# Performance work log

Hardware: AMD Instinct MI355X
Metric: run time of the kernel (lower is better)

Reference implementation:

```python
import jax, jax.numpy as jnp
import numpy as np

TEMPERATURE = 0.07
SCALE_BY_TEMPERATURE = True
N = 4096
D = 256
N_POS = 32768
CHUNK = 128  # row-chunk size for the cdist to bound the [CHUNK, N, D] temp


def setup_inputs() -> dict:
    key = jax.random.key(0)
    k1, k2, k3 = jax.random.split(key, 3)
    out = jax.random.normal(k1, (N, D), dtype=jnp.float32)
    row = jax.random.randint(k2, (N_POS,), 0, N, dtype=jnp.int32)
    col = jax.random.randint(k3, (N_POS,), 0, N, dtype=jnp.int32)
    return {"out": out, "row": row, "col": col}


def _l1_cdist(x):
    """Pairwise Manhattan distance [N, N], computed in row chunks so the
    [CHUNK, N, D] broadcast temporary stays bounded."""
    n, d = x.shape
    xr = x.reshape(n // CHUNK, CHUNK, d)

    def chunk_dist(xc):  # xc: [CHUNK, D] -> [CHUNK, N]
        return jnp.sum(jnp.abs(xc[:, None, :] - x[None, :, :]), axis=-1)

    return jax.lax.map(chunk_dist, xr).reshape(n, n)


def reference(out, row, col):
    n = out.shape[0]
    sim = -_l1_cdist(out) / TEMPERATURE                      # [N, N]
    logits_max = jax.lax.stop_gradient(jnp.max(sim, axis=1, keepdims=True))
    sim = sim - logits_max
    logits_mask = 1.0 - jnp.eye(n, dtype=sim.dtype)          # zero out self-sims
    denom = jnp.log(jnp.sum(jnp.exp(sim) * logits_mask, axis=1, keepdims=True))
    log_probs = sim - denom                                  # [N, N]
    loss = -jnp.mean(log_probs[row, col])                    # gather positive pairs
    if SCALE_BY_TEMPERATURE:
        loss = loss * TEMPERATURE
    return loss
```

## Files before the change

### kernel.cpp

```cpp
#include <hip/hip_runtime.h>
#include <math.h>

#define N 4096
#define D 256
#define NPOS 32768
#define TEMP 0.07f
#define INVT (1.0f / 0.07f)
#define BIGF 3.0e38f

#define RQ 5.5f
#define QS (255.0f / (2.0f * RQ))
#define DEQ (2.0f * RQ / 255.0f)

#define NT 64
#define NTRI (NT * (NT + 1) / 2)
#define KC 16

#define WS_PSTAT 0
#define WS_T    (2 * N * NT)
#define WS_ACC  (2 * N * NT + N)
#define WS_CNT  (2 * N * NT + N + 1)
#define WS_XQ   (2 * N * NT + N + 4)

__device__ __forceinline__ void sad_acc(unsigned a, unsigned b, unsigned& c) {
#if __has_builtin(__builtin_amdgcn_sad_u8)
    c = __builtin_amdgcn_sad_u8(a, b, c);
#else
    asm("v_sad_u8 %0, %1, %2, %0" : "+v"(c) : "v"(a), "v"(b));
#endif
}

__device__ __forceinline__ void g2l16(const unsigned* g, unsigned* l) {
    __builtin_amdgcn_global_load_lds(
        (const __attribute__((address_space(1))) unsigned*)g,
        (__attribute__((address_space(3))) unsigned*)l, 16, 0, 0);
}

__device__ __forceinline__ unsigned quant1(float v) {
    const float f = fminf(fmaxf((v + RQ) * QS, 0.0f), 255.0f);
    return (unsigned)__float2uint_rn(f);
}

__global__ __launch_bounds__(256)
void cvt_init_k(const float* __restrict__ x, unsigned* __restrict__ xqT,
                float* __restrict__ acc, unsigned* __restrict__ cnt) {
    __shared__ unsigned t[64][65];
    const int r0 = blockIdx.x * 64;
    const int tid = threadIdx.x;
#pragma unroll
    for (int k = 0; k < 16; ++k) {
        const int idx = k * 256 + tid;
        const int rr = idx >> 6;
        const int w = idx & 63;
        const float4 v = ((const float4*)x)[(size_t)(r0 + rr) * 64 + w];
        t[w][rr] = quant1(v.x) | (quant1(v.y) << 8) |
                   (quant1(v.z) << 16) | (quant1(v.w) << 24);
    }
    __syncthreads();
#pragma unroll
    for (int k = 0; k < 16; ++k) {
        const int idx = k * 256 + tid;
        const int w = idx >> 6;
        const int rr = idx & 63;
        xqT[(size_t)w * N + r0 + rr] = t[w][rr];
    }
    if (blockIdx.x == 0 && tid == 0) { *acc = 0.0f; *cnt = 0u; }
}

__global__ __launch_bounds__(64) __attribute__((amdgpu_waves_per_eu(1, 2)))
void dist_tile_k(const unsigned* __restrict__ xqT, float2* __restrict__ pstat) {
    const int tt = blockIdx.x;
    const int u_ = (NTRI - 1) - tt;
    int r = (int)((sqrtf((float)(8 * u_ + 1)) - 1.0f) * 0.5f);
    while (r * (r + 1) / 2 > u_) --r;
    while ((r + 1) * (r + 2) / 2 <= u_) ++r;
    const int bm = (NT - 1) - r;
    const int bn = (NT - 1) - (u_ - r * (r + 1) / 2);
    const bool diag = (bm == bn);

    const int lane = threadIdx.x;
    const int tx = lane & 7;
    const int ty = lane >> 3;

    __shared__ unsigned As[2][KC][64];
    __shared__ unsigned Bs[2][KC][64];

    unsigned uacc[8][8];
#pragma unroll
    for (int i = 0; i < 8; ++i)
#pragma unroll
        for (int j = 0; j < 8; ++j) uacc[i][j] = 0u;

    const int rowA0 = bm * 64;
    const int rowB0 = bn * 64;

    const int lrow = lane >> 4;
    const int lcol = (lane & 15) * 4;
    const unsigned* gA = xqT + (size_t)lrow * N + rowA0 + lcol;
    const unsigned* gB = xqT + (size_t)lrow * N + rowB0 + lcol;

#pragma unroll
    for (int q = 0; q < 4; ++q) {
        g2l16(gA + (size_t)q * 4 * N, &As[0][q * 4][0]);
        g2l16(gB + (size_t)q * 4 * N, &Bs[0][q * 4][0]);
    }
    __syncthreads();

#pragma unroll 1
    for (int chk = 0; chk < 4; ++chk) {
        const int b = chk & 1;
        if (chk < 3) {
            const unsigned* pa = gA + (size_t)(chk + 1) * 16 * N;
            const unsigned* pb = gB + (size_t)(chk + 1) * 16 * N;
            unsigned* Ad = &As[b ^ 1][0][0];
            unsigned* Bd = &Bs[b ^ 1][0][0];
#pragma unroll
            for (int q = 0; q < 4; ++q) {
                g2l16(pa + (size_t)q * 4 * N, Ad + q * 256);
                g2l16(pb + (size_t)q * 4 * N, Bd + q * 256);
            }
        }

        const unsigned* Ab = &As[b][0][0];
        const unsigned* Bb = &Bs[b][0][0];
#pragma unroll
        for (int k4 = 0; k4 < KC; ++k4) {
            const uint4 a0 = *(const uint4*)(Ab + k4 * 64 + ty * 8);
            const uint4 a1 = *(const uint4*)(Ab + k4 * 64 + ty * 8 + 4);
            const uint4 b0 = *(const uint4*)(Bb + k4 * 64 + tx * 8);
            const uint4 b1 = *(const uint4*)(Bb + k4 * 64 + tx * 8 + 4);
            const unsigned av[8] = {a0.x, a0.y, a0.z, a0.w,
                                    a1.x, a1.y, a1.z, a1.w};
            const unsigned bv[8] = {b0.x, b0.y, b0.z, b0.w,
                                    b1.x, b1.y, b1.z, b1.w};
#pragma unroll
            for (int i = 0; i < 8; ++i)
#pragma unroll
                for (int j = 0; j < 8; ++j)
                    sad_acc(av[i], bv[j], uacc[i][j]);
        }
        __syncthreads();
    }

    float acc[8][8];
#pragma unroll
    for (int i = 0; i < 8; ++i)
#pragma unroll
        for (int j = 0; j < 8; ++j)
            acc[i][j] = (float)uacc[i][j] * DEQ;

    if (diag) {
#pragma unroll
        for (int i = 0; i < 8; ++i)
#pragma unroll
            for (int j = 0; j < 8; ++j)
                if (ty * 8 + i == tx * 8 + j)
                    acc[i][j] = BIGF;
    }

#pragma unroll
    for (int i = 0; i < 8; ++i) {
        float mn = BIGF;
#pragma unroll
        for (int j = 0; j < 8; ++j) mn = fminf(mn, acc[i][j]);
        mn = fminf(mn, __shfl_xor(mn, 1, 64));
        mn = fminf(mn, __shfl_xor(mn, 2, 64));
        mn = fminf(mn, __shfl_xor(mn, 4, 64));
        float s = 0.0f;
#pragma unroll
        for (int j = 0; j < 8; ++j)
            s += __expf((mn - acc[i][j]) * INVT);
        s += __shfl_xor(s, 1, 64);
        s += __shfl_xor(s, 2, 64);
        s += __shfl_xor(s, 4, 64);
        if (tx == 0)
            pstat[(size_t)(rowA0 + ty * 8 + i) * NT + bn] = make_float2(mn, s);
    }

    if (!diag) {
#pragma unroll
        for (int j = 0; j < 8; ++j) {
            float mn = BIGF;
#pragma unroll
            for (int i = 0; i < 8; ++i) mn = fminf(mn, acc[i][j]);
            mn = fminf(mn, __shfl_xor(mn, 8, 64));
            mn = fminf(mn, __shfl_xor(mn, 16, 64));
            mn = fminf(mn, __shfl_xor(mn, 32, 64));
            float s = 0.0f;
#pragma unroll
            for (int i = 0; i < 8; ++i)
                s += __expf((mn - acc[i][j]) * INVT);
            s += __shfl_xor(s, 8, 64);
            s += __shfl_xor(s, 16, 64);
            s += __shfl_xor(s, 32, 64);
            if (ty == 0)
                pstat[(size_t)(rowB0 + tx * 8 + j) * NT + bm] =
                    make_float2(mn, s);
        }
    }
}

__global__ __launch_bounds__(256)
void row_stats_k(const float2* __restrict__ pstat, float* __restrict__ t) {
    const int r = blockIdx.x * 4 + (threadIdx.x >> 6);
    const int c = threadIdx.x & 63;
    const float2 p = pstat[(size_t)r * NT + c];
    float mn = p.x;
#pragma unroll
    for (int off = 32; off > 0; off >>= 1) mn = fminf(mn, __shfl_xor(mn, off, 64));
    float s = p.y * __expf((mn - p.x) * INVT);
#pragma unroll
    for (int off = 32; off > 0; off >>= 1) s += __shfl_xor(s, off, 64);
    if (c == 0) t[r] = TEMP * __logf(s) - mn;
}

__global__ __launch_bounds__(256)
void pair_fin_k(const float* __restrict__ x, const int* __restrict__ row,
                const int* __restrict__ col, const float* __restrict__ t,
                float* __restrict__ acc, unsigned* __restrict__ cnt,
                float* __restrict__ out) {
    const int lane = threadIdx.x & 63;
    const int wave = threadIdx.x >> 6;
    const int p0 = (blockIdx.x * 4 + wave) * 8;

    int rp[8], cp[8];
#pragma unroll
    for (int i = 0; i < 8; ++i) { rp[i] = row[p0 + i]; cp[i] = col[p0 + i]; }
    float4 a[8], b[8];
#pragma unroll
    for (int i = 0; i < 8; ++i) {
        a[i] = *(const float4*)&x[(size_t)rp[i] * D + lane * 4];
        b[i] = *(const float4*)&x[(size_t)cp[i] * D + lane * 4];
    }
    float wsum = 0.0f;
#pragma unroll
    for (int i = 0; i < 8; ++i) {
        float d = fabsf(a[i].x - b[i].x) + fabsf(a[i].y - b[i].y) +
                  fabsf(a[i].z - b[i].z) + fabsf(a[i].w - b[i].w);
#pragma unroll
        for (int off = 32; off > 0; off >>= 1) d += __shfl_xor(d, off, 64);
        if (lane == 0) wsum += d + t[rp[i]];
    }

    __shared__ float bs[4];
    if (lane == 0) bs[wave] = wsum;
    __syncthreads();
    if (threadIdx.x == 0) {
        const float tot = bs[0] + bs[1] + bs[2] + bs[3];
        atomicAdd(acc, tot);
        __threadfence();
        const unsigned tk = atomicAdd(cnt, 1u);
        if (tk == (unsigned)(gridDim.x - 1)) {
            const float v = atomicAdd(acc, 0.0f);
            out[0] = v * (1.0f / (float)NPOS);
        }
    }
}

extern "C" void kernel_launch(void* const* d_in, const int* in_sizes, int n_in,
                              void* d_out, int out_size, void* d_ws, size_t ws_size,
                              hipStream_t stream) {
    const float* x = (const float*)d_in[0];
    const int* row = (const int*)d_in[1];
    const int* col = (const int*)d_in[2];
    float* ws = (float*)d_ws;
    float* out = (float*)d_out;
    unsigned* xqT = (unsigned*)(ws + WS_XQ);
    float* acc = ws + WS_ACC;
    unsigned* cnt = (unsigned*)(ws + WS_CNT);

    cvt_init_k<<<N / 64, 256, 0, stream>>>(x, xqT, acc, cnt);

    dist_tile_k<<<NTRI, 64, 0, stream>>>(xqT, (float2*)(ws + WS_PSTAT));

    row_stats_k<<<N / 4, 256, 0, stream>>>((const float2*)(ws + WS_PSTAT), ws + WS_T);

    pair_fin_k<<<NPOS / 32, 256, 0, stream>>>(x, row, col, ws + WS_T, acc, cnt, out);
}
```

Before: 135.6 us.

## Pack four tile wavefronts per block and double-buffer LDS register fragments

The distance tile kernel now runs four independent 64x64 triangle tiles per 256-thread block, one per wavefront, each with its own LDS buffers. The launch bound changes from waves_per_eu(1,2) to launch_bounds(256,2). The inner k loop is also software-pipelined so the next k-slice's LDS fragments load while the current SAD accumulation runs. This aims to cut block scheduling overhead and hide LDS latency, at the cost of more registers per thread and four times the LDS per block. NTRI (2080) divides evenly by 4, and the block-wide __syncthreads now couple the four waves, which can stall the faster ones.

```diff
diff --git a/kernel.cpp b/kernel.cpp
--- a/kernel.cpp
+++ b/kernel.cpp
@@ -67,9 +67,11 @@
     if (blockIdx.x == 0 && tid == 0) { *acc = 0.0f; *cnt = 0u; }
 }
 
-__global__ __launch_bounds__(64) __attribute__((amdgpu_waves_per_eu(1, 2)))
+__global__ __launch_bounds__(256, 2)
 void dist_tile_k(const unsigned* __restrict__ xqT, float2* __restrict__ pstat) {
-    const int tt = blockIdx.x;
+    const int lane = threadIdx.x & 63;
+    const int w = threadIdx.x >> 6;
+    const int tt = blockIdx.x * 4 + w;
     const int u_ = (NTRI - 1) - tt;
     int r = (int)((sqrtf((float)(8 * u_ + 1)) - 1.0f) * 0.5f);
     while (r * (r + 1) / 2 > u_) --r;
@@ -78,12 +80,11 @@
     const int bn = (NT - 1) - (u_ - r * (r + 1) / 2);
     const bool diag = (bm == bn);
 
-    const int lane = threadIdx.x;
     const int tx = lane & 7;
     const int ty = lane >> 3;
 
-    __shared__ unsigned As[2][KC][64];
-    __shared__ unsigned Bs[2][KC][64];
+    __shared__ unsigned As[4][2][KC][64];
+    __shared__ unsigned Bs[4][2][KC][64];
 
     unsigned uacc[8][8];
 #pragma unroll
@@ -101,19 +102,27 @@
 
 #pragma unroll
     for (int q = 0; q < 4; ++q) {
-        g2l16(gA + (size_t)q * 4 * N, &As[0][q * 4][0]);
-        g2l16(gB + (size_t)q * 4 * N, &Bs[0][q * 4][0]);
+        g2l16(gA + (size_t)q * 4 * N, &As[w][0][q * 4][0]);
+        g2l16(gB + (size_t)q * 4 * N, &Bs[w][0][q * 4][0]);
     }
     __syncthreads();
 
 #pragma unroll 1
     for (int chk = 0; chk < 4; ++chk) {
         const int b = chk & 1;
+        const unsigned* Ab = &As[w][b][0][0];
+        const unsigned* Bb = &Bs[w][b][0][0];
+
+        uint4 a0_0 = *(const uint4*)(Ab + ty * 8);
+        uint4 a1_0 = *(const uint4*)(Ab + ty * 8 + 4);
+        uint4 b0_0 = *(const uint4*)(Bb + tx * 8);
+        uint4 b1_0 = *(const uint4*)(Bb + tx * 8 + 4);
+
         if (chk < 3) {
             const unsigned* pa = gA + (size_t)(chk + 1) * 16 * N;
             const unsigned* pb = gB + (size_t)(chk + 1) * 16 * N;
-            unsigned* Ad = &As[b ^ 1][0][0];
-            unsigned* Bd = &Bs[b ^ 1][0][0];
+            unsigned* Ad = &As[w][b ^ 1][0][0];
+            unsigned* Bd = &Bs[w][b ^ 1][0][0];
 #pragma unroll
             for (int q = 0; q < 4; ++q) {
                 g2l16(pa + (size_t)q * 4 * N, Ad + q * 256);
@@ -121,23 +130,41 @@
             }
         }
 
-        const unsigned* Ab = &As[b][0][0];
-        const unsigned* Bb = &Bs[b][0][0];
-#pragma unroll
-        for (int k4 = 0; k4 < KC; ++k4) {
-            const uint4 a0 = *(const uint4*)(Ab + k4 * 64 + ty * 8);
-            const uint4 a1 = *(const uint4*)(Ab + k4 * 64 + ty * 8 + 4);
-            const uint4 b0 = *(const uint4*)(Bb + k4 * 64 + tx * 8);
-            const uint4 b1 = *(const uint4*)(Bb + k4 * 64 + tx * 8 + 4);
-            const unsigned av[8] = {a0.x, a0.y, a0.z, a0.w,
-                                    a1.x, a1.y, a1.z, a1.w};
-            const unsigned bv[8] = {b0.x, b0.y, b0.z, b0.w,
-                                    b1.x, b1.y, b1.z, b1.w};
-#pragma unroll
-            for (int i = 0; i < 8; ++i)
-#pragma unroll
-                for (int j = 0; j < 8; ++j)
-                    sad_acc(av[i], bv[j], uacc[i][j]);
+#pragma unroll
+        for (int k2 = 0; k2 < 8; ++k2) {
+            const int k4 = 2 * k2;
+            const uint4 a0_1 = *(const uint4*)(Ab + (k4 + 1) * 64 + ty * 8);
+            const uint4 a1_1 = *(const uint4*)(Ab + (k4 + 1) * 64 + ty * 8 + 4);
+            const uint4 b0_1 = *(const uint4*)(Bb + (k4 + 1) * 64 + tx * 8);
+            const uint4 b1_1 = *(const uint4*)(Bb + (k4 + 1) * 64 + tx * 8 + 4);
+            {
+                const unsigned av[8] = {a0_0.x, a0_0.y, a0_0.z, a0_0.w,
+                                        a1_0.x, a1_0.y, a1_0.z, a1_0.w};
+                const unsigned bv[8] = {b0_0.x, b0_0.y, b0_0.z, b0_0.w,
+                                        b1_0.x, b1_0.y, b1_0.z, b1_0.w};
+#pragma unroll
+                for (int i = 0; i < 8; ++i)
+#pragma unroll
+                    for (int j = 0; j < 8; ++j)
+                        sad_acc(av[i], bv[j], uacc[i][j]);
+            }
+            if (k2 < 7) {
+                a0_0 = *(const uint4*)(Ab + (k4 + 2) * 64 + ty * 8);
+                a1_0 = *(const uint4*)(Ab + (k4 + 2) * 64 + ty * 8 + 4);
+                b0_0 = *(const uint4*)(Bb + (k4 + 2) * 64 + tx * 8);
+                b1_0 = *(const uint4*)(Bb + (k4 + 2) * 64 + tx * 8 + 4);
+            }
+            {
+                const unsigned av[8] = {a0_1.x, a0_1.y, a0_1.z, a0_1.w,
+                                        a1_1.x, a1_1.y, a1_1.z, a1_1.w};
+                const unsigned bv[8] = {b0_1.x, b0_1.y, b0_1.z, b0_1.w,
+                                        b1_1.x, b1_1.y, b1_1.z, b1_1.w};
+#pragma unroll
+                for (int i = 0; i < 8; ++i)
+#pragma unroll
+                    for (int j = 0; j < 8; ++j)
+                        sad_acc(av[i], bv[j], uacc[i][j]);
+            }
         }
         __syncthreads();
     }
@@ -271,7 +298,7 @@
 
     cvt_init_k<<<N / 64, 256, 0, stream>>>(x, xqT, acc, cnt);
 
-    dist_tile_k<<<NTRI, 64, 0, stream>>>(xqT, (float2*)(ws + WS_PSTAT));
+    dist_tile_k<<<NTRI / 4, 256, 0, stream>>>(xqT, (float2*)(ws + WS_PSTAT));
 
     row_stats_k<<<N / 4, 256, 0, stream>>>((const float2*)(ws + WS_PSTAT), ws + WS_T);
 
```

Measured after the change: 134.1 us. Within noise of the previous version (-1.1%).

## Split-K distance tiles across two waves and fuse row stats into pair kernel

Applied to the files above, without the earlier changes.

The distance tile kernel now runs two waves per block, each covering half of the K dimension (32 packed words) with its own LDS slice and no double buffering. Partial SAD accumulators are merged through shared memory before the epilogue. The separate row_stats kernel is removed and its per-row min/logsumexp reduction is recomputed inside pair_fin for every sampled pair, saving a launch but redoing the reduction per pair. The goal is more parallelism and latency hiding in the main kernel, at the cost of an LDS merge step, an idle second wave during the epilogue, and redundant row-stat work.

```diff
diff --git a/kernel.cpp b/kernel.cpp
--- a/kernel.cpp
+++ b/kernel.cpp
@@ -17,10 +17,9 @@
 #define KC 16
 
 #define WS_PSTAT 0
-#define WS_T    (2 * N * NT)
-#define WS_ACC  (2 * N * NT + N)
-#define WS_CNT  (2 * N * NT + N + 1)
-#define WS_XQ   (2 * N * NT + N + 4)
+#define WS_ACC  (2 * N * NT)
+#define WS_CNT  (2 * N * NT + 1)
+#define WS_XQ   (2 * N * NT + 4)
 
 __device__ __forceinline__ void sad_acc(unsigned a, unsigned b, unsigned& c) {
 #if __has_builtin(__builtin_amdgcn_sad_u8)
@@ -67,7 +66,7 @@
     if (blockIdx.x == 0 && tid == 0) { *acc = 0.0f; *cnt = 0u; }
 }
 
-__global__ __launch_bounds__(64) __attribute__((amdgpu_waves_per_eu(1, 2)))
+__global__ __launch_bounds__(128)
 void dist_tile_k(const unsigned* __restrict__ xqT, float2* __restrict__ pstat) {
     const int tt = blockIdx.x;
     const int u_ = (NTRI - 1) - tt;
@@ -78,12 +77,15 @@
     const int bn = (NT - 1) - (u_ - r * (r + 1) / 2);
     const bool diag = (bm == bn);
 
-    const int lane = threadIdx.x;
+    const int tid = threadIdx.x;
+    const int lane = tid & 63;
+    const int w = tid >> 6;
     const int tx = lane & 7;
     const int ty = lane >> 3;
 
-    __shared__ unsigned As[2][KC][64];
-    __shared__ unsigned Bs[2][KC][64];
+    __shared__ unsigned Sl[4][KC][64];
+    unsigned* Aw = &Sl[w][0][0];
+    unsigned* Bw = &Sl[2 + w][0][0];
 
     unsigned uacc[8][8];
 #pragma unroll
@@ -94,41 +96,26 @@
     const int rowA0 = bm * 64;
     const int rowB0 = bn * 64;
 
-    const int lrow = lane >> 4;
-    const int lcol = (lane & 15) * 4;
-    const unsigned* gA = xqT + (size_t)lrow * N + rowA0 + lcol;
-    const unsigned* gB = xqT + (size_t)lrow * N + rowB0 + lcol;
-
-#pragma unroll
-    for (int q = 0; q < 4; ++q) {
-        g2l16(gA + (size_t)q * 4 * N, &As[0][q * 4][0]);
-        g2l16(gB + (size_t)q * 4 * N, &Bs[0][q * 4][0]);
-    }
-    __syncthreads();
-
-#pragma unroll 1
-    for (int chk = 0; chk < 4; ++chk) {
-        const int b = chk & 1;
-        if (chk < 3) {
-            const unsigned* pa = gA + (size_t)(chk + 1) * 16 * N;
-            const unsigned* pb = gB + (size_t)(chk + 1) * 16 * N;
-            unsigned* Ad = &As[b ^ 1][0][0];
-            unsigned* Bd = &Bs[b ^ 1][0][0];
-#pragma unroll
-            for (int q = 0; q < 4; ++q) {
-                g2l16(pa + (size_t)q * 4 * N, Ad + q * 256);
-                g2l16(pb + (size_t)q * 4 * N, Bd + q * 256);
-            }
-        }
-
-        const unsigned* Ab = &As[b][0][0];
-        const unsigned* Bb = &Bs[b][0][0];
+    const unsigned* gA =
+        xqT + (size_t)(32 * w + (lane >> 4)) * N + rowA0 + (lane & 15) * 4;
+    const unsigned* gB =
+        xqT + (size_t)(32 * w + (lane >> 4)) * N + rowB0 + (lane & 15) * 4;
+
+#pragma unroll
+    for (int c2 = 0; c2 < 2; ++c2) {
+        const size_t base = (size_t)(16 * c2) * N;
+#pragma unroll
+        for (int q = 0; q < 4; ++q) {
+            g2l16(gA + base + (size_t)q * 4 * N, Aw + q * 256);
+            g2l16(gB + base + (size_t)q * 4 * N, Bw + q * 256);
+        }
+        asm volatile("s_waitcnt vmcnt(0)" ::: "memory");
 #pragma unroll
         for (int k4 = 0; k4 < KC; ++k4) {
-            const uint4 a0 = *(const uint4*)(Ab + k4 * 64 + ty * 8);
-            const uint4 a1 = *(const uint4*)(Ab + k4 * 64 + ty * 8 + 4);
-            const uint4 b0 = *(const uint4*)(Bb + k4 * 64 + tx * 8);
-            const uint4 b1 = *(const uint4*)(Bb + k4 * 64 + tx * 8 + 4);
+            const uint4 a0 = *(const uint4*)(Aw + k4 * 64 + ty * 8);
+            const uint4 a1 = *(const uint4*)(Aw + k4 * 64 + ty * 8 + 4);
+            const uint4 b0 = *(const uint4*)(Bw + k4 * 64 + tx * 8);
+            const uint4 b1 = *(const uint4*)(Bw + k4 * 64 + tx * 8 + 4);
             const unsigned av[8] = {a0.x, a0.y, a0.z, a0.w,
                                     a1.x, a1.y, a1.z, a1.w};
             const unsigned bv[8] = {b0.x, b0.y, b0.z, b0.w,
@@ -139,7 +126,29 @@
                 for (int j = 0; j < 8; ++j)
                     sad_acc(av[i], bv[j], uacc[i][j]);
         }
-        __syncthreads();
+    }
+
+    unsigned* mb = &Sl[0][0][0];
+    __syncthreads();
+    if (w == 1) {
+#pragma unroll
+        for (int k = 0; k < 16; ++k) {
+            const int i = k >> 1, p = (k & 1) * 4;
+            const int slot = (k + lane) & 15;
+            *(uint4*)(mb + lane * 64 + slot * 4) =
+                make_uint4(uacc[i][p], uacc[i][p + 1],
+                           uacc[i][p + 2], uacc[i][p + 3]);
+        }
+    }
+    __syncthreads();
+    if (w == 1) return;
+#pragma unroll
+    for (int k = 0; k < 16; ++k) {
+        const int i = k >> 1, p = (k & 1) * 4;
+        const int slot = (k + lane) & 15;
+        const uint4 v = *(const uint4*)(mb + lane * 64 + slot * 4);
+        uacc[i][p] += v.x; uacc[i][p + 1] += v.y;
+        uacc[i][p + 2] += v.z; uacc[i][p + 3] += v.w;
     }
 
     float acc[8][8];
@@ -201,22 +210,8 @@
 }
 
 __global__ __launch_bounds__(256)
-void row_stats_k(const float2* __restrict__ pstat, float* __restrict__ t) {
-    const int r = blockIdx.x * 4 + (threadIdx.x >> 6);
-    const int c = threadIdx.x & 63;
-    const float2 p = pstat[(size_t)r * NT + c];
-    float mn = p.x;
-#pragma unroll
-    for (int off = 32; off > 0; off >>= 1) mn = fminf(mn, __shfl_xor(mn, off, 64));
-    float s = p.y * __expf((mn - p.x) * INVT);
-#pragma unroll
-    for (int off = 32; off > 0; off >>= 1) s += __shfl_xor(s, off, 64);
-    if (c == 0) t[r] = TEMP * __logf(s) - mn;
-}
-
-__global__ __launch_bounds__(256)
 void pair_fin_k(const float* __restrict__ x, const int* __restrict__ row,
-                const int* __restrict__ col, const float* __restrict__ t,
+                const int* __restrict__ col, const float2* __restrict__ pstat,
                 float* __restrict__ acc, unsigned* __restrict__ cnt,
                 float* __restrict__ out) {
     const int lane = threadIdx.x & 63;
@@ -239,7 +234,15 @@
                   fabsf(a[i].z - b[i].z) + fabsf(a[i].w - b[i].w);
 #pragma unroll
         for (int off = 32; off > 0; off >>= 1) d += __shfl_xor(d, off, 64);
-        if (lane == 0) wsum += d + t[rp[i]];
+        const float2 p = pstat[(size_t)rp[i] * NT + lane];
+        float mn = p.x;
+#pragma unroll
+        for (int off = 32; off > 0; off >>= 1)
+            mn = fminf(mn, __shfl_xor(mn, off, 64));
+        float s = p.y * __expf((mn - p.x) * INVT);
+#pragma unroll
+        for (int off = 32; off > 0; off >>= 1) s += __shfl_xor(s, off, 64);
+        if (lane == 0) wsum += d + (TEMP * __logf(s) - mn);
     }
 
     __shared__ float bs[4];
@@ -271,9 +274,9 @@
 
     cvt_init_k<<<N / 64, 256, 0, stream>>>(x, xqT, acc, cnt);
 
-    dist_tile_k<<<NTRI, 64, 0, stream>>>(xqT, (float2*)(ws + WS_PSTAT));
-
-    row_stats_k<<<N / 4, 256, 0, stream>>>((const float2*)(ws + WS_PSTAT), ws + WS_T);
-
-    pair_fin_k<<<NPOS / 32, 256, 0, stream>>>(x, row, col, ws + WS_T, acc, cnt, out);
-}
+    dist_tile_k<<<NTRI, 128, 0, stream>>>(xqT, (float2*)(ws + WS_PSTAT));
+
+    pair_fin_k<<<NPOS / 32, 256, 0, stream>>>(x, row, col,
+                                              (const float2*)(ws + WS_PSTAT),
+                                              acc, cnt, out);
+}
```

Result: faster. 129.4 us (-4.6%).
